# Kernel optimization log

Measured on AMD Instinct MI355X. Metric: run time of the kernel, lower is better.

Reference implementation:

```python
import jax, jax.numpy as jnp
import numpy as np

MD = 20          # max_displacement
TEMP = 1e-4      # softmax temperature
B, C, H, W = 4, 64, 112, 112


def setup_inputs() -> dict:
    key = jax.random.key(0)
    k1, k2 = jax.random.split(key)
    in1 = jax.random.normal(k1, (B, C, H, W), dtype=jnp.float32)
    in2 = jax.random.normal(k2, (B, C, H, W), dtype=jnp.float32)
    return {"in1": in1, "in2": in2}


def reference(in1, in2):
    b, c, h, w = in1.shape
    # F.normalize(x, dim=1): x / max(||x||_2, eps)
    def l2n(x):
        return x / jnp.maximum(jnp.linalg.norm(x, axis=1, keepdims=True), 1e-12)
    in1 = l2n(in1)
    in2 = l2n(in2)

    pad = jnp.pad(in2, ((0, 0), (0, 0), (MD, MD), (MD, MD)))

    d = jnp.arange(-MD, MD + 1)
    dx, dy = jnp.meshgrid(d, d, indexing="ij")  # torch.meshgrid default 'ij'
    dx = dx.reshape(-1)  # [K] with K = (2*MD+1)^2
    dy = dy.reshape(-1)

    def sim_one(dxi, dyi):
        # shifted window of padded in2, same spatial size as in1
        sl = jax.lax.dynamic_slice(pad, (0, 0, MD + dxi, MD + dyi), (b, c, h, w))
        return jnp.sum(in1 * sl, axis=1)  # [B,H,W]

    sim = jax.vmap(sim_one)(dx, dy)          # [K,B,H,W]
    sim = jnp.transpose(sim, (1, 0, 2, 3))   # [B,K,H,W] cost volume

    weights = jax.nn.softmax(sim / TEMP, axis=1)  # softmax over displacements
    guide = jnp.stack((dx, dy), axis=-1).astype(jnp.float32)  # [K,2]
    # flow[b,d,h,w] = sum_k weights[b,k,h,w] * guide[k,d]
    flow = jnp.einsum("bkhw,kd->bdhw", weights, guide)
    return flow
```

## Files before the change

kernel.cpp:

```cpp
#include <hip/hip_runtime.h>

#define BB 4
#define CC 64
#define HH 112
#define WW 112
#define MD 20
#define KD 41
#define S2 14426.950408f
#define NPIX (BB*HH*WW)
#define NT 10
#define ROW2 (NT*2*2*64*8)
#define IN2S_BYTES ((size_t)BB*HH*ROW2*2)
#define NEG (-60000.0f)

typedef _Float16 half8   __attribute__((ext_vector_type(8)));
typedef float    f32x4   __attribute__((ext_vector_type(4)));
typedef unsigned short ushort8 __attribute__((ext_vector_type(8)));

static __device__ __forceinline__ float fmax_f(float a, float b) { return a > b ? a : b; }
static __device__ __forceinline__ unsigned short f2h_bits(float x) {
    _Float16 h = (_Float16)x;
    return __builtin_bit_cast(unsigned short, h);
}
static __device__ __forceinline__ float h2f(unsigned short s) {
    return (float)__builtin_bit_cast(_Float16, s);
}
static __device__ __forceinline__ f32x4 vmax4(f32x4 a, f32x4 b) {
    f32x4 r;
    #pragma unroll
    for (int k = 0; k < 4; ++k) r[k] = a[k] > b[k] ? a[k] : b[k];
    return r;
}
static __device__ __forceinline__ f32x4 vexp4(f32x4 d) {
    f32x4 r;
    #pragma unroll
    for (int k = 0; k < 4; ++k) r[k] = __builtin_amdgcn_exp2f(d[k]);
    return r;
}
static __device__ __forceinline__ f32x4 mfma16(half8 a, half8 b, f32x4 c) {
    return __builtin_amdgcn_mfma_f32_16x16x32_f16(a, b, c, 0, 0, 0);
}

__global__ __launch_bounds__(256) void pack_kernel(const float* __restrict__ in2,
                                                   unsigned short* __restrict__ in2s) {
    int wid = blockIdx.x*4 + (threadIdx.x >> 6);
    int lane = threadIdx.x & 63;
    int tau = wid % NT;
    int bh  = wid / NT;
    int b = bh / HH, h = bh % HH;
    int n = lane & 15, q = lane >> 4;
    int col = 16*tau + n - MD;
    bool ok = (col >= 0 && col < WW);
    int colc = ok ? col : 0;
    const float* src = in2 + ((size_t)(b*CC)*HH + h)*WW + colc;

    float x[16];
    float ss = 0.f;
    #pragma unroll
    for (int ks = 0; ks < 2; ++ks)
        #pragma unroll
        for (int j = 0; j < 8; ++j) {
            float v = ok ? src[(size_t)(32*ks + 8*q + j)*(HH*WW)] : 0.f;
            x[ks*8 + j] = v;
            ss += v*v;
        }
    ss += __shfl_xor(ss, 16);
    ss += __shfl_xor(ss, 32);
    float iv = 1.0f / fmax_f(__builtin_sqrtf(ss), 1e-12f);

    unsigned short* base = in2s + (size_t)(b*HH + h)*ROW2;
    #pragma unroll
    for (int ks = 0; ks < 2; ++ks) {
        ushort8 hb, lb;
        #pragma unroll
        for (int j = 0; j < 8; ++j) {
            float v = x[ks*8 + j] * iv;
            unsigned short vh = f2h_bits(v);
            hb[j] = vh;
            lb[j] = f2h_bits((v - h2f(vh)) * 4096.0f);
        }
        *(ushort8*)(base + (size_t)((tau*4 + ks*2 + 0)*64 + lane)*8) = hb;
        *(ushort8*)(base + (size_t)((tau*4 + ks*2 + 1)*64 + lane)*8) = lb;
    }
}

__global__ __launch_bounds__(448) void corr_kernel(const float* __restrict__ in1,
                                                   const unsigned short* __restrict__ in2s,
                                                   float* __restrict__ part) {
    int gid = blockIdx.x;
    int xcd  = gid & 7;
    int slot = gid >> 3;
    int hloc = slot % 56;
    int g    = slot / 56;
    int b    = xcd >> 1;
    int h    = (xcd & 1)*56 + hloc;
    int wt   = threadIdx.x >> 6;
    int lane = threadIdx.x & 63;
    int n = lane & 15, q = lane >> 4;
    int m0 = 4*q;
    int wA = wt*16 + n;

    const float* a_src = in1 + ((size_t)(b*CC)*HH + h)*WW + wA;
    float x[16];
    float ss = 0.f;
    #pragma unroll
    for (int ks = 0; ks < 2; ++ks)
        #pragma unroll
        for (int j = 0; j < 8; ++j) {
            float v = a_src[(size_t)(32*ks + 8*q + j)*(HH*WW)];
            x[ks*8 + j] = v;
            ss += v*v;
        }
    ss += __shfl_xor(ss, 16);
    ss += __shfl_xor(ss, 32);
    float i1 = 1.0f / fmax_f(__builtin_sqrtf(ss), 1e-12f);
    half8 aH[2], aL[2];
    #pragma unroll
    for (int ks = 0; ks < 2; ++ks)
        #pragma unroll
        for (int j = 0; j < 8; ++j) {
            float v = x[ks*8 + j] * i1;
            _Float16 vh = (_Float16)v;
            aH[ks][j] = vh;
            aL[ks][j] = (_Float16)((v - (float)vh) * 4096.0f);
        }

    f32x4 NM20; bool v0b[4], v2b[4], v3b[4];
    #pragma unroll
    for (int r = 0; r < 4; ++r) {
        int nm = n - (m0 + r);
        NM20[r] = (float)(nm - 20);
        v0b[r] = (nm >= 0);
        v2b[r] = (nm <= 8);
        v3b[r] = (nm <= -8);
    }

    f32x4 SM = {NEG,NEG,NEG,NEG}, SL = {0.f,0.f,0.f,0.f};
    f32x4 SSX = {0.f,0.f,0.f,0.f}, SSY = {0.f,0.f,0.f,0.f};

    int glo = g*14;
    int ghi = glo + 14 < KD ? glo + 14 : KD;
    int lo = glo > (MD - h) ? glo : (MD - h);
    int hi0 = HH + MD - h;
    int hi = ghi < hi0 ? ghi : hi0;
    if (hi < lo) { lo = ghi; hi = ghi; }

    for (int dxi = lo; dxi < hi; ++dxi) {
        const unsigned short* rb = in2s + (size_t)(b*HH + (h + dxi - MD))*ROW2;
        half8 bf[4][4];
        #pragma unroll
        for (int oi = 0; oi < 4; ++oi) {
            const half8* fp = (const half8*)(rb + (size_t)((wt + oi)*4*64 + lane)*8);
            bf[oi][0] = fp[0];
            bf[oi][1] = fp[64];
            bf[oi][2] = fp[128];
            bf[oi][3] = fp[192];
        }
        f32x4 sv[4];
        #pragma unroll
        for (int oi = 0; oi < 4; ++oi) {
            f32x4 a0 = {0.f,0.f,0.f,0.f}, a1 = {0.f,0.f,0.f,0.f};
            a0 = mfma16(aH[0], bf[oi][0], a0);
            a1 = mfma16(aH[0], bf[oi][1], a1);
            a1 = mfma16(aL[0], bf[oi][0], a1);
            a0 = mfma16(aH[1], bf[oi][2], a0);
            a1 = mfma16(aH[1], bf[oi][3], a1);
            a1 = mfma16(aL[1], bf[oi][2], a1);
            sv[oi] = a0*S2 + a1*(S2/4096.0f);
        }
        f32x4 V0, V1 = sv[1], V2, V3;
        #pragma unroll
        for (int r = 0; r < 4; ++r) {
            V0[r] = v0b[r] ? sv[0][r] : NEG;
            V2[r] = v2b[r] ? sv[2][r] : NEG;
            V3[r] = v3b[r] ? sv[3][r] : NEG;
        }
        f32x4 MN = vmax4(vmax4(SM, V0), vmax4(V1, vmax4(V2, V3)));
        f32x4 ER = vexp4(SM - MN);
        f32x4 E0 = vexp4(V0 - MN);
        f32x4 E1 = vexp4(V1 - MN);
        f32x4 E2 = vexp4(V2 - MN);
        f32x4 E3 = vexp4(V3 - MN);
        f32x4 SUM = (E0 + E1) + (E2 + E3);
        f32x4 TT  = E1 + E2*2.0f + E3*3.0f;
        float dxf = (float)(dxi - MD);
        SL  = SL *ER + SUM;
        SSX = SSX*ER + SUM*dxf;
        SSY = SSY*ER + (TT*16.0f + NM20*SUM);
        SM  = MN;
    }

    int miss = (lo - glo) + (ghi - hi);
    if (miss > 0) {
        float sdx = 0.f;
        for (int d = glo; d < lo; ++d)  sdx += (float)(d - MD);
        for (int d = hi; d < ghi; ++d)  sdx += (float)(d - MD);
        float cnt = (float)miss * (float)KD;
        f32x4 Z = {0.f,0.f,0.f,0.f};
        f32x4 MN = vmax4(SM, Z);
        f32x4 ER = vexp4(SM - MN);
        f32x4 E0 = vexp4(Z  - MN);
        SL  = SL *ER + E0*cnt;
        SSX = SSX*ER + E0*((float)KD*sdx);
        SSY = SSY*ER;
        SM  = MN;
    }

    #pragma unroll
    for (int off = 1; off < 16; off <<= 1) {
        f32x4 M2, L2, X2, Y2;
        #pragma unroll
        for (int k = 0; k < 4; ++k) {
            M2[k] = __shfl_xor(SM[k],  off);
            L2[k] = __shfl_xor(SL[k],  off);
            X2[k] = __shfl_xor(SSX[k], off);
            Y2[k] = __shfl_xor(SSY[k], off);
        }
        f32x4 MN = vmax4(SM, M2);
        f32x4 EA = vexp4(SM - MN);
        f32x4 EB = vexp4(M2 - MN);
        SL  = SL *EA + L2*EB;
        SSX = SSX*EA + X2*EB;
        SSY = SSY*EA + Y2*EB;
        SM  = MN;
    }

    if (n == 0) {
        #pragma unroll
        for (int r = 0; r < 4; ++r) {
            int w = wt*16 + m0 + r;
            int pix = (b*HH + h)*WW + w;
            float* p = &part[(size_t)(g*NPIX + pix)*4];
            p[0] = SM[r]; p[1] = SL[r]; p[2] = SSX[r]; p[3] = SSY[r];
        }
    }
}

__global__ __launch_bounds__(256) void merge_kernel(const float* __restrict__ part,
                                                    float* __restrict__ out) {
    int idx = blockIdx.x*256 + threadIdx.x;
    if (idx >= NPIX) return;
    const float* p0 = &part[(size_t)idx*4];
    const float* p1 = &part[(size_t)(NPIX + idx)*4];
    const float* p2 = &part[(size_t)(2*NPIX + idx)*4];
    float M = fmax_f(fmax_f(p0[0], p1[0]), p2[0]);
    float e0 = __builtin_amdgcn_exp2f(p0[0] - M);
    float e1 = __builtin_amdgcn_exp2f(p1[0] - M);
    float e2 = __builtin_amdgcn_exp2f(p2[0] - M);
    float L  = p0[1]*e0 + p1[1]*e1 + p2[1]*e2;
    float SX = p0[2]*e0 + p1[2]*e1 + p2[2]*e2;
    float SY = p0[3]*e0 + p1[3]*e1 + p2[3]*e2;
    int b = idx / (HH*WW), rem = idx % (HH*WW);
    out[(b*2 + 0)*(HH*WW) + rem] = SX / L;
    out[(b*2 + 1)*(HH*WW) + rem] = SY / L;
}

extern "C" void kernel_launch(void* const* d_in, const int* in_sizes, int n_in,
                              void* d_out, int out_size, void* d_ws, size_t ws_size,
                              hipStream_t stream) {
    const float* in1 = (const float*)d_in[0];
    const float* in2 = (const float*)d_in[1];
    float* out = (float*)d_out;
    unsigned short* in2s = (unsigned short*)d_ws;
    float* part = (float*)((char*)d_ws + IN2S_BYTES);

    pack_kernel <<<1120, 256, 0, stream>>>(in2, in2s);
    corr_kernel <<<1344, 448, 0, stream>>>(in1, in2s, part);
    merge_kernel<<<(NPIX+255)/256, 256, 0, stream>>>(part, out);
}
```

Before: 157.3 us.

## Fuse pack, correlation and merge into one persistent cooperative kernel

Replaces the three separate launches with a single cooperative kernel of 256 blocks that packs in2, runs the correlation, and merges partials, separated by grid-wide syncs. The correlation work is also restructured so each wave handles two adjacent 16-column tiles and shares the overlapping in2 fragment loads (5 loads instead of 8 for two tiles). This aims to remove launch gaps and redundant global loads. The cost is grid.sync overhead, a fixed persistent grid that may underuse CUs or leave work imbalanced, and higher register pressure from the doubled accumulators.

```diff
diff --git a/kernel.cpp b/kernel.cpp
--- a/kernel.cpp
+++ b/kernel.cpp
@@ -1,4 +1,7 @@
 #include <hip/hip_runtime.h>
+#include <hip/hip_cooperative_groups.h>
+
+namespace cg = cooperative_groups;
 
 #define BB 4
 #define CC 64
@@ -12,6 +15,7 @@
 #define ROW2 (NT*2*2*64*8)
 #define IN2S_BYTES ((size_t)BB*HH*ROW2*2)
 #define NEG (-60000.0f)
+#define NBLK 256
 
 typedef _Float16 half8   __attribute__((ext_vector_type(8)));
 typedef float    f32x4   __attribute__((ext_vector_type(4)));
@@ -41,18 +45,16 @@
     return __builtin_amdgcn_mfma_f32_16x16x32_f16(a, b, c, 0, 0, 0);
 }
 
-__global__ __launch_bounds__(256) void pack_kernel(const float* __restrict__ in2,
-                                                   unsigned short* __restrict__ in2s) {
-    int wid = blockIdx.x*4 + (threadIdx.x >> 6);
-    int lane = threadIdx.x & 63;
+static __device__ __forceinline__ void pack_unit(int wid, int lane,
+                                                 const float* __restrict__ in2,
+                                                 unsigned short* __restrict__ in2s) {
     int tau = wid % NT;
     int bh  = wid / NT;
     int b = bh / HH, h = bh % HH;
     int n = lane & 15, q = lane >> 4;
     int col = 16*tau + n - MD;
     bool ok = (col >= 0 && col < WW);
-    int colc = ok ? col : 0;
-    const float* src = in2 + ((size_t)(b*CC)*HH + h)*WW + colc;
+    const float* src = in2 + ((size_t)(b*CC)*HH + h)*WW + (ok ? col : 0);
 
     float x[16];
     float ss = 0.f;
@@ -84,175 +86,216 @@
     }
 }
 
-__global__ __launch_bounds__(448) void corr_kernel(const float* __restrict__ in1,
-                                                   const unsigned short* __restrict__ in2s,
-                                                   float* __restrict__ part) {
-    int gid = blockIdx.x;
-    int xcd  = gid & 7;
-    int slot = gid >> 3;
-    int hloc = slot % 56;
-    int g    = slot / 56;
-    int b    = xcd >> 1;
-    int h    = (xcd & 1)*56 + hloc;
-    int wt   = threadIdx.x >> 6;
+__global__ __launch_bounds__(512, 2) void fused_kernel(const float* __restrict__ in1,
+                                                       const float* __restrict__ in2,
+                                                       float* __restrict__ out,
+                                                       unsigned short* __restrict__ in2s,
+                                                       float* __restrict__ part) {
+    cg::grid_group grid = cg::this_grid();
+    int blk  = blockIdx.x;
+    int wv   = threadIdx.x >> 6;
     int lane = threadIdx.x & 63;
-    int n = lane & 15, q = lane >> 4;
-    int m0 = 4*q;
-    int wA = wt*16 + n;
-
-    const float* a_src = in1 + ((size_t)(b*CC)*HH + h)*WW + wA;
-    float x[16];
-    float ss = 0.f;
-    #pragma unroll
-    for (int ks = 0; ks < 2; ++ks)
-        #pragma unroll
-        for (int j = 0; j < 8; ++j) {
-            float v = a_src[(size_t)(32*ks + 8*q + j)*(HH*WW)];
-            x[ks*8 + j] = v;
-            ss += v*v;
-        }
-    ss += __shfl_xor(ss, 16);
-    ss += __shfl_xor(ss, 32);
-    float i1 = 1.0f / fmax_f(__builtin_sqrtf(ss), 1e-12f);
-    half8 aH[2], aL[2];
-    #pragma unroll
-    for (int ks = 0; ks < 2; ++ks)
-        #pragma unroll
-        for (int j = 0; j < 8; ++j) {
-            float v = x[ks*8 + j] * i1;
-            _Float16 vh = (_Float16)v;
-            aH[ks][j] = vh;
-            aL[ks][j] = (_Float16)((v - (float)vh) * 4096.0f);
-        }
-
-    f32x4 NM20; bool v0b[4], v2b[4], v3b[4];
-    #pragma unroll
-    for (int r = 0; r < 4; ++r) {
-        int nm = n - (m0 + r);
-        NM20[r] = (float)(nm - 20);
-        v0b[r] = (nm >= 0);
-        v2b[r] = (nm <= 8);
-        v3b[r] = (nm <= -8);
-    }
-
-    f32x4 SM = {NEG,NEG,NEG,NEG}, SL = {0.f,0.f,0.f,0.f};
-    f32x4 SSX = {0.f,0.f,0.f,0.f}, SSY = {0.f,0.f,0.f,0.f};
-
-    int glo = g*14;
-    int ghi = glo + 14 < KD ? glo + 14 : KD;
-    int lo = glo > (MD - h) ? glo : (MD - h);
-    int hi0 = HH + MD - h;
-    int hi = ghi < hi0 ? ghi : hi0;
-    if (hi < lo) { lo = ghi; hi = ghi; }
-
-    for (int dxi = lo; dxi < hi; ++dxi) {
-        const unsigned short* rb = in2s + (size_t)(b*HH + (h + dxi - MD))*ROW2;
-        half8 bf[4][4];
-        #pragma unroll
-        for (int oi = 0; oi < 4; ++oi) {
-            const half8* fp = (const half8*)(rb + (size_t)((wt + oi)*4*64 + lane)*8);
-            bf[oi][0] = fp[0];
-            bf[oi][1] = fp[64];
-            bf[oi][2] = fp[128];
-            bf[oi][3] = fp[192];
-        }
-        f32x4 sv[4];
-        #pragma unroll
-        for (int oi = 0; oi < 4; ++oi) {
-            f32x4 a0 = {0.f,0.f,0.f,0.f}, a1 = {0.f,0.f,0.f,0.f};
-            a0 = mfma16(aH[0], bf[oi][0], a0);
-            a1 = mfma16(aH[0], bf[oi][1], a1);
-            a1 = mfma16(aL[0], bf[oi][0], a1);
-            a0 = mfma16(aH[1], bf[oi][2], a0);
-            a1 = mfma16(aH[1], bf[oi][3], a1);
-            a1 = mfma16(aL[1], bf[oi][2], a1);
-            sv[oi] = a0*S2 + a1*(S2/4096.0f);
-        }
-        f32x4 V0, V1 = sv[1], V2, V3;
+
+    for (int u = blk*8 + wv; u < BB*HH*NT; u += NBLK*8)
+        pack_unit(u, lane, in2, in2s);
+
+    __threadfence();
+    grid.sync();
+
+    {
+        int slab = blk & 7;
+        int sblk = blk >> 3;
+        int b = slab >> 1;
+        int n = lane & 15, q = lane >> 4;
+        int m0 = 4*q;
+
+        f32x4 NM20; bool v0b[4], v2b[4], v3b[4];
         #pragma unroll
         for (int r = 0; r < 4; ++r) {
-            V0[r] = v0b[r] ? sv[0][r] : NEG;
-            V2[r] = v2b[r] ? sv[2][r] : NEG;
-            V3[r] = v3b[r] ? sv[3][r] : NEG;
+            int nm = n - (m0 + r);
+            NM20[r] = (float)(nm - 20);
+            v0b[r] = (nm >= 0);
+            v2b[r] = (nm <= 8);
+            v3b[r] = (nm <= -8);
         }
-        f32x4 MN = vmax4(vmax4(SM, V0), vmax4(V1, vmax4(V2, V3)));
-        f32x4 ER = vexp4(SM - MN);
-        f32x4 E0 = vexp4(V0 - MN);
-        f32x4 E1 = vexp4(V1 - MN);
-        f32x4 E2 = vexp4(V2 - MN);
-        f32x4 E3 = vexp4(V3 - MN);
-        f32x4 SUM = (E0 + E1) + (E2 + E3);
-        f32x4 TT  = E1 + E2*2.0f + E3*3.0f;
-        float dxf = (float)(dxi - MD);
-        SL  = SL *ER + SUM;
-        SSX = SSX*ER + SUM*dxf;
-        SSY = SSY*ER + (TT*16.0f + NM20*SUM);
-        SM  = MN;
-    }
-
-    int miss = (lo - glo) + (ghi - hi);
-    if (miss > 0) {
-        float sdx = 0.f;
-        for (int d = glo; d < lo; ++d)  sdx += (float)(d - MD);
-        for (int d = hi; d < ghi; ++d)  sdx += (float)(d - MD);
-        float cnt = (float)miss * (float)KD;
-        f32x4 Z = {0.f,0.f,0.f,0.f};
-        f32x4 MN = vmax4(SM, Z);
-        f32x4 ER = vexp4(SM - MN);
-        f32x4 E0 = vexp4(Z  - MN);
-        SL  = SL *ER + E0*cnt;
-        SSX = SSX*ER + E0*((float)KD*sdx);
-        SSY = SSY*ER;
-        SM  = MN;
-    }
-
-    #pragma unroll
-    for (int off = 1; off < 16; off <<= 1) {
-        f32x4 M2, L2, X2, Y2;
-        #pragma unroll
-        for (int k = 0; k < 4; ++k) {
-            M2[k] = __shfl_xor(SM[k],  off);
-            L2[k] = __shfl_xor(SL[k],  off);
-            X2[k] = __shfl_xor(SSX[k], off);
-            Y2[k] = __shfl_xor(SSY[k], off);
-        }
-        f32x4 MN = vmax4(SM, M2);
-        f32x4 EA = vexp4(SM - MN);
-        f32x4 EB = vexp4(M2 - MN);
-        SL  = SL *EA + L2*EB;
-        SSX = SSX*EA + X2*EB;
-        SSY = SSY*EA + Y2*EB;
-        SM  = MN;
-    }
-
-    if (n == 0) {
-        #pragma unroll
-        for (int r = 0; r < 4; ++r) {
-            int w = wt*16 + m0 + r;
-            int pix = (b*HH + h)*WW + w;
-            float* p = &part[(size_t)(g*NPIX + pix)*4];
-            p[0] = SM[r]; p[1] = SL[r]; p[2] = SSX[r]; p[3] = SSY[r];
+
+        for (int local = sblk*8 + wv; local < 672; local += 256) {
+            int hloc = local % 56;
+            int rest = local / 56;
+            int g = rest >> 2;
+            int u = rest & 3;
+            int h = (slab & 1)*56 + hloc;
+            int ntile = (u < 3) ? 2 : 1;
+            int q0 = 2*u;
+            int NQ = (u < 3) ? 5 : 4;
+
+            half8 aH[2][2], aL[2][2];
+            #pragma unroll
+            for (int t = 0; t < 2; ++t) {
+                if (t >= ntile) break;
+                int wA = (q0 + t)*16 + n;
+                const float* a_src = in1 + ((size_t)(b*CC)*HH + h)*WW + wA;
+                float x[16], ss = 0.f;
+                #pragma unroll
+                for (int ks = 0; ks < 2; ++ks)
+                    #pragma unroll
+                    for (int j = 0; j < 8; ++j) {
+                        float v = a_src[(size_t)(32*ks + 8*q + j)*(HH*WW)];
+                        x[ks*8 + j] = v;
+                        ss += v*v;
+                    }
+                ss += __shfl_xor(ss, 16);
+                ss += __shfl_xor(ss, 32);
+                float i1 = 1.0f / fmax_f(__builtin_sqrtf(ss), 1e-12f);
+                #pragma unroll
+                for (int ks = 0; ks < 2; ++ks)
+                    #pragma unroll
+                    for (int j = 0; j < 8; ++j) {
+                        float v = x[ks*8 + j] * i1;
+                        _Float16 vh = (_Float16)v;
+                        aH[t][ks][j] = vh;
+                        aL[t][ks][j] = (_Float16)((v - (float)vh) * 4096.0f);
+                    }
+            }
+
+            f32x4 SM[2], SL[2], SSX[2], SSY[2];
+            #pragma unroll
+            for (int t = 0; t < 2; ++t) {
+                SM[t] = f32x4{NEG,NEG,NEG,NEG}; SL[t] = f32x4{0.f,0.f,0.f,0.f};
+                SSX[t] = f32x4{0.f,0.f,0.f,0.f}; SSY[t] = f32x4{0.f,0.f,0.f,0.f};
+            }
+
+            int glo = g*14;
+            int ghi = glo + 14 < KD ? glo + 14 : KD;
+            int lo = glo > (MD - h) ? glo : (MD - h);
+            int hi0 = HH + MD - h;
+            int hi = ghi < hi0 ? ghi : hi0;
+            if (hi < lo) { lo = ghi; hi = ghi; }
+
+            for (int dxi = lo; dxi < hi; ++dxi) {
+                const unsigned short* rb = in2s + (size_t)(b*HH + (h + dxi - MD))*ROW2
+                                         + (size_t)q0*2048 + (size_t)lane*8;
+                half8 bq[5][4];
+                #pragma unroll
+                for (int j = 0; j < 5; ++j) {
+                    if (j >= NQ) break;
+                    const half8* fp = (const half8*)(rb + (size_t)j*2048);
+                    bq[j][0] = fp[0];
+                    bq[j][1] = fp[64];
+                    bq[j][2] = fp[128];
+                    bq[j][3] = fp[192];
+                }
+                float dxf = (float)(dxi - MD);
+                #pragma unroll
+                for (int t = 0; t < 2; ++t) {
+                    if (t >= ntile) break;
+                    f32x4 sv[4];
+                    #pragma unroll
+                    for (int oi = 0; oi < 4; ++oi) {
+                        const half8* f = bq[t + oi];
+                        f32x4 a0 = {0.f,0.f,0.f,0.f}, a1 = {0.f,0.f,0.f,0.f};
+                        a0 = mfma16(aH[t][0], f[0], a0);
+                        a1 = mfma16(aH[t][0], f[1], a1);
+                        a1 = mfma16(aL[t][0], f[0], a1);
+                        a0 = mfma16(aH[t][1], f[2], a0);
+                        a1 = mfma16(aH[t][1], f[3], a1);
+                        a1 = mfma16(aL[t][1], f[2], a1);
+                        sv[oi] = a0*S2 + a1*(S2/4096.0f);
+                    }
+                    f32x4 V0, V1 = sv[1], V2, V3;
+                    #pragma unroll
+                    for (int r = 0; r < 4; ++r) {
+                        V0[r] = v0b[r] ? sv[0][r] : NEG;
+                        V2[r] = v2b[r] ? sv[2][r] : NEG;
+                        V3[r] = v3b[r] ? sv[3][r] : NEG;
+                    }
+                    f32x4 MN = vmax4(vmax4(SM[t], V0), vmax4(V1, vmax4(V2, V3)));
+                    f32x4 ER = vexp4(SM[t] - MN);
+                    f32x4 E0 = vexp4(V0 - MN);
+                    f32x4 E1 = vexp4(V1 - MN);
+                    f32x4 E2 = vexp4(V2 - MN);
+                    f32x4 E3 = vexp4(V3 - MN);
+                    f32x4 SUM = (E0 + E1) + (E2 + E3);
+                    f32x4 TT  = E1 + E2*2.0f + E3*3.0f;
+                    SL[t]  = SL[t] *ER + SUM;
+                    SSX[t] = SSX[t]*ER + SUM*dxf;
+                    SSY[t] = SSY[t]*ER + (TT*16.0f + NM20*SUM);
+                    SM[t]  = MN;
+                }
+            }
+
+            int miss = (lo - glo) + (ghi - hi);
+            if (miss > 0) {
+                float sdx = 0.f;
+                for (int d = glo; d < lo; ++d) sdx += (float)(d - MD);
+                for (int d = hi; d < ghi; ++d) sdx += (float)(d - MD);
+                float cnt = (float)miss * (float)KD;
+                #pragma unroll
+                for (int t = 0; t < 2; ++t) {
+                    if (t >= ntile) break;
+                    f32x4 Z = {0.f,0.f,0.f,0.f};
+                    f32x4 MN = vmax4(SM[t], Z);
+                    f32x4 ER = vexp4(SM[t] - MN);
+                    f32x4 E0 = vexp4(Z - MN);
+                    SL[t]  = SL[t] *ER + E0*cnt;
+                    SSX[t] = SSX[t]*ER + E0*((float)KD*sdx);
+                    SSY[t] = SSY[t]*ER;
+                    SM[t]  = MN;
+                }
+            }
+
+            #pragma unroll
+            for (int t = 0; t < 2; ++t) {
+                if (t >= ntile) break;
+                #pragma unroll
+                for (int off = 1; off < 16; off <<= 1) {
+                    f32x4 M2, L2, X2, Y2;
+                    #pragma unroll
+                    for (int k = 0; k < 4; ++k) {
+                        M2[k] = __shfl_xor(SM[t][k],  off);
+                        L2[k] = __shfl_xor(SL[t][k],  off);
+                        X2[k] = __shfl_xor(SSX[t][k], off);
+                        Y2[k] = __shfl_xor(SSY[t][k], off);
+                    }
+                    f32x4 MN = vmax4(SM[t], M2);
+                    f32x4 EA = vexp4(SM[t] - MN);
+                    f32x4 EB = vexp4(M2 - MN);
+                    SL[t]  = SL[t] *EA + L2*EB;
+                    SSX[t] = SSX[t]*EA + X2*EB;
+                    SSY[t] = SSY[t]*EA + Y2*EB;
+                    SM[t]  = MN;
+                }
+                if (n == 0) {
+                    #pragma unroll
+                    for (int r = 0; r < 4; ++r) {
+                        int w = (q0 + t)*16 + m0 + r;
+                        int pix = (b*HH + h)*WW + w;
+                        float* p = &part[(size_t)(g*NPIX + pix)*4];
+                        p[0] = SM[t][r]; p[1] = SL[t][r]; p[2] = SSX[t][r]; p[3] = SSY[t][r];
+                    }
+                }
+            }
         }
     }
-}
-
-__global__ __launch_bounds__(256) void merge_kernel(const float* __restrict__ part,
-                                                    float* __restrict__ out) {
-    int idx = blockIdx.x*256 + threadIdx.x;
-    if (idx >= NPIX) return;
-    const float* p0 = &part[(size_t)idx*4];
-    const float* p1 = &part[(size_t)(NPIX + idx)*4];
-    const float* p2 = &part[(size_t)(2*NPIX + idx)*4];
-    float M = fmax_f(fmax_f(p0[0], p1[0]), p2[0]);
-    float e0 = __builtin_amdgcn_exp2f(p0[0] - M);
-    float e1 = __builtin_amdgcn_exp2f(p1[0] - M);
-    float e2 = __builtin_amdgcn_exp2f(p2[0] - M);
-    float L  = p0[1]*e0 + p1[1]*e1 + p2[1]*e2;
-    float SX = p0[2]*e0 + p1[2]*e1 + p2[2]*e2;
-    float SY = p0[3]*e0 + p1[3]*e1 + p2[3]*e2;
-    int b = idx / (HH*WW), rem = idx % (HH*WW);
-    out[(b*2 + 0)*(HH*WW) + rem] = SX / L;
-    out[(b*2 + 1)*(HH*WW) + rem] = SY / L;
+
+    __threadfence();
+    grid.sync();
+
+    for (int idx = blk*512 + (int)threadIdx.x; idx < NPIX; idx += NBLK*512) {
+        const float* p0 = &part[(size_t)idx*4];
+        const float* p1 = &part[(size_t)(NPIX + idx)*4];
+        const float* p2 = &part[(size_t)(2*NPIX + idx)*4];
+        float M = fmax_f(fmax_f(p0[0], p1[0]), p2[0]);
+        float e0 = __builtin_amdgcn_exp2f(p0[0] - M);
+        float e1 = __builtin_amdgcn_exp2f(p1[0] - M);
+        float e2 = __builtin_amdgcn_exp2f(p2[0] - M);
+        float L  = p0[1]*e0 + p1[1]*e1 + p2[1]*e2;
+        float SX = p0[2]*e0 + p1[2]*e1 + p2[2]*e2;
+        float SY = p0[3]*e0 + p1[3]*e1 + p2[3]*e2;
+        int b = idx / (HH*WW), rem = idx % (HH*WW);
+        out[(b*2 + 0)*(HH*WW) + rem] = SX / L;
+        out[(b*2 + 1)*(HH*WW) + rem] = SY / L;
+    }
 }
 
 extern "C" void kernel_launch(void* const* d_in, const int* in_sizes, int n_in,
@@ -264,7 +307,7 @@
     unsigned short* in2s = (unsigned short*)d_ws;
     float* part = (float*)((char*)d_ws + IN2S_BYTES);
 
-    pack_kernel <<<1120, 256, 0, stream>>>(in2, in2s);
-    corr_kernel <<<1344, 448, 0, stream>>>(in1, in2s, part);
-    merge_kernel<<<(NPIX+255)/256, 256, 0, stream>>>(part, out);
-}
+    void* args[] = { (void*)&in1, (void*)&in2, (void*)&out, (void*)&in2s, (void*)&part };
+    hipLaunchCooperativeKernel((void*)fused_kernel, dim3(NBLK), dim3(512),
+                               args, 0, stream);
+}
```

Result: slower. 317.9 us (+102.1%).

## Skip low-order correction MFMAs for displacements far below running max; tile pack via LDS

Applied to the files above, without the earlier changes.

The correlation loop now computes only the high-half fp16 product first. It runs the four low-order correction MFMAs and the softmax update only when some lane's candidate is within a margin of a per-row running max, shared across lanes by shuffles. With temperature 1e-4, displacements far below the max contribute essentially nothing, so skipping them is meant to save matrix work and exponentials. The cost is wave-level branching and an approximation whose error depends on the margin. The pack kernel is also restructured to stage a 64-column channel tile in shared memory for coalesced loads and a cheaper norm computation.

```diff
diff --git a/kernel.cpp b/kernel.cpp
--- a/kernel.cpp
+++ b/kernel.cpp
@@ -12,6 +12,7 @@
 #define ROW2 (NT*2*2*64*8)
 #define IN2S_BYTES ((size_t)BB*HH*ROW2*2)
 #define NEG (-60000.0f)
+#define MARGIN 32.0f
 
 typedef _Float16 half8   __attribute__((ext_vector_type(8)));
 typedef float    f32x4   __attribute__((ext_vector_type(4)));
@@ -43,41 +44,48 @@
 
 __global__ __launch_bounds__(256) void pack_kernel(const float* __restrict__ in2,
                                                    unsigned short* __restrict__ in2s) {
-    int wid = blockIdx.x*4 + (threadIdx.x >> 6);
-    int lane = threadIdx.x & 63;
-    int tau = wid % NT;
-    int bh  = wid / NT;
+    __shared__ float tile[CC][65];
+    __shared__ float sinv[64];
+    int bid = blockIdx.x;
+    int side = bid & 1;
+    int bh = bid >> 1;
     int b = bh / HH, h = bh % HH;
+    int cb = side ? 48 : 0;
+    int t = threadIdx.x;
+    const float* src = in2 + ((size_t)b*CC*HH + h)*WW;
+
+    for (int i = t; i < CC*64; i += 256) {
+        int c = i >> 6, w = i & 63;
+        int col = cb + w;
+        tile[c][w] = (col < WW) ? src[(size_t)c*(HH*WW) + col] : 0.f;
+    }
+    __syncthreads();
+    if (t < 64) {
+        float s = 0.f;
+        #pragma unroll
+        for (int c = 0; c < CC; ++c) { float x = tile[c][t]; s += x*x; }
+        sinv[t] = 1.0f / fmax_f(__builtin_sqrtf(s), 1e-12f);
+    }
+    __syncthreads();
+
+    int wv = t >> 6, lane = t & 63;
     int n = lane & 15, q = lane >> 4;
-    int col = 16*tau + n - MD;
-    bool ok = (col >= 0 && col < WW);
-    int colc = ok ? col : 0;
-    const float* src = in2 + ((size_t)(b*CC)*HH + h)*WW + colc;
-
-    float x[16];
-    float ss = 0.f;
-    #pragma unroll
-    for (int ks = 0; ks < 2; ++ks)
+    unsigned short* base = in2s + (size_t)bh*ROW2;
+    for (int u = wv; u < 10; u += 4) {
+        int tl = u >> 1, ks = u & 1;
+        int tau = 5*side + tl;
+        int col = 16*tau + n - MD;
+        bool ok = (col >= 0 && col < WW);
+        int lc = ok ? (col - cb) : 0;
+        float iv = ok ? sinv[lc] : 0.f;
+        ushort8 hb, lb;
         #pragma unroll
         for (int j = 0; j < 8; ++j) {
-            float v = ok ? src[(size_t)(32*ks + 8*q + j)*(HH*WW)] : 0.f;
-            x[ks*8 + j] = v;
-            ss += v*v;
-        }
-    ss += __shfl_xor(ss, 16);
-    ss += __shfl_xor(ss, 32);
-    float iv = 1.0f / fmax_f(__builtin_sqrtf(ss), 1e-12f);
-
-    unsigned short* base = in2s + (size_t)(b*HH + h)*ROW2;
-    #pragma unroll
-    for (int ks = 0; ks < 2; ++ks) {
-        ushort8 hb, lb;
-        #pragma unroll
-        for (int j = 0; j < 8; ++j) {
-            float v = x[ks*8 + j] * iv;
-            unsigned short vh = f2h_bits(v);
-            hb[j] = vh;
-            lb[j] = f2h_bits((v - h2f(vh)) * 4096.0f);
+            int c = 32*ks + 8*q + j;
+            float x = tile[c][lc] * iv;
+            unsigned short xh = f2h_bits(x);
+            hb[j] = xh;
+            lb[j] = f2h_bits((x - h2f(xh)) * 4096.0f);
         }
         *(ushort8*)(base + (size_t)((tau*4 + ks*2 + 0)*64 + lane)*8) = hb;
         *(ushort8*)(base + (size_t)((tau*4 + ks*2 + 1)*64 + lane)*8) = lb;
@@ -137,6 +145,7 @@
 
     f32x4 SM = {NEG,NEG,NEG,NEG}, SL = {0.f,0.f,0.f,0.f};
     f32x4 SSX = {0.f,0.f,0.f,0.f}, SSY = {0.f,0.f,0.f,0.f};
+    f32x4 PM = {NEG,NEG,NEG,NEG};
 
     int glo = g*14;
     int ghi = glo + 14 < KD ? glo + 14 : KD;
@@ -146,48 +155,66 @@
     if (hi < lo) { lo = ghi; hi = ghi; }
 
     for (int dxi = lo; dxi < hi; ++dxi) {
-        const unsigned short* rb = in2s + (size_t)(b*HH + (h + dxi - MD))*ROW2;
-        half8 bf[4][4];
+        const unsigned short* rb = in2s + (size_t)(b*HH + (h + dxi - MD))*ROW2
+                                 + (size_t)lane*8;
+        half8 bh0[4], bh1[4];
         #pragma unroll
         for (int oi = 0; oi < 4; ++oi) {
-            const half8* fp = (const half8*)(rb + (size_t)((wt + oi)*4*64 + lane)*8);
-            bf[oi][0] = fp[0];
-            bf[oi][1] = fp[64];
-            bf[oi][2] = fp[128];
-            bf[oi][3] = fp[192];
-        }
-        f32x4 sv[4];
+            const half8* fp = (const half8*)(rb + (size_t)(wt + oi)*2048);
+            bh0[oi] = fp[0];
+            bh1[oi] = fp[128];
+        }
+        f32x4 ah[4];
         #pragma unroll
         for (int oi = 0; oi < 4; ++oi) {
-            f32x4 a0 = {0.f,0.f,0.f,0.f}, a1 = {0.f,0.f,0.f,0.f};
-            a0 = mfma16(aH[0], bf[oi][0], a0);
-            a1 = mfma16(aH[0], bf[oi][1], a1);
-            a1 = mfma16(aL[0], bf[oi][0], a1);
-            a0 = mfma16(aH[1], bf[oi][2], a0);
-            a1 = mfma16(aH[1], bf[oi][3], a1);
-            a1 = mfma16(aL[1], bf[oi][2], a1);
-            sv[oi] = a0*S2 + a1*(S2/4096.0f);
-        }
-        f32x4 V0, V1 = sv[1], V2, V3;
-        #pragma unroll
-        for (int r = 0; r < 4; ++r) {
-            V0[r] = v0b[r] ? sv[0][r] : NEG;
-            V2[r] = v2b[r] ? sv[2][r] : NEG;
-            V3[r] = v3b[r] ? sv[3][r] : NEG;
-        }
-        f32x4 MN = vmax4(vmax4(SM, V0), vmax4(V1, vmax4(V2, V3)));
-        f32x4 ER = vexp4(SM - MN);
-        f32x4 E0 = vexp4(V0 - MN);
-        f32x4 E1 = vexp4(V1 - MN);
-        f32x4 E2 = vexp4(V2 - MN);
-        f32x4 E3 = vexp4(V3 - MN);
-        f32x4 SUM = (E0 + E1) + (E2 + E3);
-        f32x4 TT  = E1 + E2*2.0f + E3*3.0f;
+            f32x4 a0 = {0.f,0.f,0.f,0.f};
+            a0 = mfma16(aH[0], bh0[oi], a0);
+            a0 = mfma16(aH[1], bh1[oi], a0);
+            ah[oi] = a0 * S2;
+        }
         float dxf = (float)(dxi - MD);
-        SL  = SL *ER + SUM;
-        SSX = SSX*ER + SUM*dxf;
-        SSY = SSY*ER + (TT*16.0f + NM20*SUM);
-        SM  = MN;
+        bool anyPass = false;
+        #pragma unroll
+        for (int oi = 0; oi < 4; ++oi) {
+            f32x4 Vh;
+            #pragma unroll
+            for (int r = 0; r < 4; ++r) {
+                bool ok = (oi == 0) ? v0b[r] : (oi == 1) ? true
+                        : (oi == 2) ? v2b[r] : v3b[r];
+                Vh[r] = ok ? ah[oi][r] : NEG;
+            }
+            f32x4 d = Vh - PM;
+            float tm = fmax_f(fmax_f(d[0], d[1]), fmax_f(d[2], d[3]));
+            if (__any(tm > -MARGIN)) {
+                anyPass = true;
+                const half8* fp = (const half8*)(rb + (size_t)(wt + oi)*2048);
+                half8 bl0 = fp[64], bl1 = fp[192];
+                f32x4 a1 = {0.f,0.f,0.f,0.f};
+                a1 = mfma16(aH[0], bl0, a1);
+                a1 = mfma16(aL[0], bh0[oi], a1);
+                a1 = mfma16(aH[1], bl1, a1);
+                a1 = mfma16(aL[1], bh1[oi], a1);
+                f32x4 sv = Vh + a1*(S2/4096.0f);
+                f32x4 MN = vmax4(SM, sv);
+                f32x4 ER = vexp4(SM - MN);
+                f32x4 E  = vexp4(sv - MN);
+                float c16 = (float)(16*oi);
+                SL  = SL *ER + E;
+                SSX = SSX*ER + E*dxf;
+                SSY = SSY*ER + E*(NM20 + c16);
+                SM  = MN;
+            }
+        }
+        if (anyPass) {
+            PM = SM;
+            #pragma unroll
+            for (int off = 1; off < 16; off <<= 1) {
+                f32x4 P2;
+                #pragma unroll
+                for (int k = 0; k < 4; ++k) P2[k] = __shfl_xor(PM[k], off);
+                PM = vmax4(PM, P2);
+            }
+        }
     }
 
     int miss = (lo - glo) + (ghi - hi);
@@ -264,7 +291,7 @@
     unsigned short* in2s = (unsigned short*)d_ws;
     float* part = (float*)((char*)d_ws + IN2S_BYTES);
 
-    pack_kernel <<<1120, 256, 0, stream>>>(in2, in2s);
+    pack_kernel <<<BB*HH*2, 256, 0, stream>>>(in2, in2s);
     corr_kernel <<<1344, 448, 0, stream>>>(in1, in2s, part);
     merge_kernel<<<(NPIX+255)/256, 256, 0, stream>>>(part, out);
 }
```

Result: slower. 185.0 us (+17.6%).

## Fuse merge into corr kernel via per-tile atomic counter, drop merge launch

Applied to the files above, without the earlier changes.

Removes the separate merge kernel. Each corr wave writes its partial softmax stats, fences, and atomically increments a per-(b,h,wave-tile) counter; the last of the three displacement groups merges the partials and writes the flow output. Counters are zeroed in the pack kernel, which now uses 64-thread blocks. This saves a kernel launch and a global pass over the partial buffer, at the cost of atomics, fences and a tail of extra work on the last-arriving wave.

```diff
diff --git a/kernel.cpp b/kernel.cpp
--- a/kernel.cpp
+++ b/kernel.cpp
@@ -12,6 +12,7 @@
 #define ROW2 (NT*2*2*64*8)
 #define IN2S_BYTES ((size_t)BB*HH*ROW2*2)
 #define NEG (-60000.0f)
+#define NTILE (BB*HH*7)
 
 typedef _Float16 half8   __attribute__((ext_vector_type(8)));
 typedef float    f32x4   __attribute__((ext_vector_type(4)));
@@ -41,18 +42,22 @@
     return __builtin_amdgcn_mfma_f32_16x16x32_f16(a, b, c, 0, 0, 0);
 }
 
-__global__ __launch_bounds__(256) void pack_kernel(const float* __restrict__ in2,
-                                                   unsigned short* __restrict__ in2s) {
-    int wid = blockIdx.x*4 + (threadIdx.x >> 6);
-    int lane = threadIdx.x & 63;
+__global__ __launch_bounds__(64) void pack_kernel(const float* __restrict__ in2,
+                                                  unsigned short* __restrict__ in2s,
+                                                  unsigned int* __restrict__ cnt) {
+    int wid = blockIdx.x;
+    int lane = threadIdx.x;
+    if (wid < (NTILE + 63)/64) {
+        int i = wid*64 + lane;
+        if (i < NTILE) cnt[i] = 0u;
+    }
     int tau = wid % NT;
     int bh  = wid / NT;
     int b = bh / HH, h = bh % HH;
     int n = lane & 15, q = lane >> 4;
     int col = 16*tau + n - MD;
     bool ok = (col >= 0 && col < WW);
-    int colc = ok ? col : 0;
-    const float* src = in2 + ((size_t)(b*CC)*HH + h)*WW + colc;
+    const float* src = in2 + ((size_t)(b*CC)*HH + h)*WW + (ok ? col : 0);
 
     float x[16];
     float ss = 0.f;
@@ -86,7 +91,9 @@
 
 __global__ __launch_bounds__(448) void corr_kernel(const float* __restrict__ in1,
                                                    const unsigned short* __restrict__ in2s,
-                                                   float* __restrict__ part) {
+                                                   float* __restrict__ part,
+                                                   unsigned int* __restrict__ cnt,
+                                                   float* __restrict__ out) {
     int gid = blockIdx.x;
     int xcd  = gid & 7;
     int slot = gid >> 3;
@@ -195,12 +202,12 @@
         float sdx = 0.f;
         for (int d = glo; d < lo; ++d)  sdx += (float)(d - MD);
         for (int d = hi; d < ghi; ++d)  sdx += (float)(d - MD);
-        float cnt = (float)miss * (float)KD;
+        float cntf = (float)miss * (float)KD;
         f32x4 Z = {0.f,0.f,0.f,0.f};
         f32x4 MN = vmax4(SM, Z);
         f32x4 ER = vexp4(SM - MN);
         f32x4 E0 = vexp4(Z  - MN);
-        SL  = SL *ER + E0*cnt;
+        SL  = SL *ER + E0*cntf;
         SSX = SSX*ER + E0*((float)KD*sdx);
         SSY = SSY*ER;
         SM  = MN;
@@ -225,34 +232,40 @@
         SM  = MN;
     }
 
+    int tile = (b*HH + h)*7 + wt;
     if (n == 0) {
         #pragma unroll
         for (int r = 0; r < 4; ++r) {
             int w = wt*16 + m0 + r;
             int pix = (b*HH + h)*WW + w;
-            float* p = &part[(size_t)(g*NPIX + pix)*4];
-            p[0] = SM[r]; p[1] = SL[r]; p[2] = SSX[r]; p[3] = SSY[r];
-        }
-    }
-}
-
-__global__ __launch_bounds__(256) void merge_kernel(const float* __restrict__ part,
-                                                    float* __restrict__ out) {
-    int idx = blockIdx.x*256 + threadIdx.x;
-    if (idx >= NPIX) return;
-    const float* p0 = &part[(size_t)idx*4];
-    const float* p1 = &part[(size_t)(NPIX + idx)*4];
-    const float* p2 = &part[(size_t)(2*NPIX + idx)*4];
-    float M = fmax_f(fmax_f(p0[0], p1[0]), p2[0]);
-    float e0 = __builtin_amdgcn_exp2f(p0[0] - M);
-    float e1 = __builtin_amdgcn_exp2f(p1[0] - M);
-    float e2 = __builtin_amdgcn_exp2f(p2[0] - M);
-    float L  = p0[1]*e0 + p1[1]*e1 + p2[1]*e2;
-    float SX = p0[2]*e0 + p1[2]*e1 + p2[2]*e2;
-    float SY = p0[3]*e0 + p1[3]*e1 + p2[3]*e2;
-    int b = idx / (HH*WW), rem = idx % (HH*WW);
-    out[(b*2 + 0)*(HH*WW) + rem] = SX / L;
-    out[(b*2 + 1)*(HH*WW) + rem] = SY / L;
+            f32x4 rec = {SM[r], SL[r], SSX[r], SSY[r]};
+            *(f32x4*)&part[(size_t)(g*NPIX + pix)*4] = rec;
+        }
+    }
+
+    __threadfence();
+    unsigned int old = 0u;
+    if (lane == 0) old = atomicAdd(&cnt[tile], 1u);
+    old = __shfl(old, 0);
+    if (old == 2u) {
+        __threadfence();
+        if (lane < 16) {
+            int w = wt*16 + lane;
+            int pix = (b*HH + h)*WW + w;
+            f32x4 p0 = *(const f32x4*)&part[(size_t)(0*NPIX + pix)*4];
+            f32x4 p1 = *(const f32x4*)&part[(size_t)(1*NPIX + pix)*4];
+            f32x4 p2 = *(const f32x4*)&part[(size_t)(2*NPIX + pix)*4];
+            float M = fmax_f(fmax_f(p0[0], p1[0]), p2[0]);
+            float e0 = __builtin_amdgcn_exp2f(p0[0] - M);
+            float e1 = __builtin_amdgcn_exp2f(p1[0] - M);
+            float e2 = __builtin_amdgcn_exp2f(p2[0] - M);
+            float L  = p0[1]*e0 + p1[1]*e1 + p2[1]*e2;
+            float SX = p0[2]*e0 + p1[2]*e1 + p2[2]*e2;
+            float SY = p0[3]*e0 + p1[3]*e1 + p2[3]*e2;
+            out[((b*2 + 0)*HH + h)*WW + w] = SX / L;
+            out[((b*2 + 1)*HH + h)*WW + w] = SY / L;
+        }
+    }
 }
 
 extern "C" void kernel_launch(void* const* d_in, const int* in_sizes, int n_in,
@@ -263,8 +276,8 @@
     float* out = (float*)d_out;
     unsigned short* in2s = (unsigned short*)d_ws;
     float* part = (float*)((char*)d_ws + IN2S_BYTES);
-
-    pack_kernel <<<1120, 256, 0, stream>>>(in2, in2s);
-    corr_kernel <<<1344, 448, 0, stream>>>(in1, in2s, part);
-    merge_kernel<<<(NPIX+255)/256, 256, 0, stream>>>(part, out);
-}
+    unsigned int* cnt = (unsigned int*)(part + (size_t)3*NPIX*4);
+
+    pack_kernel<<<BB*HH*NT, 64, 0, stream>>>(in2, in2s, cnt);
+    corr_kernel<<<1344, 448, 0, stream>>>(in1, in2s, part, cnt, out);
+}
```

New measurement: 418.4 us. +166.0%, slower.
